# Optimization experiments

Measured on AMD Instinct MI355X. Metric: run time of the kernel, lower is better.

The kernel has to match this reference:

```python
import jax, jax.numpy as jnp
import numpy as np

B, L, M = 8192, 64, 64
LOCAL_DIM, MAX_UP, MAX_DN = 4, 64, 64


def setup_inputs() -> dict:
    key = jax.random.key(0)
    k1, k2 = jax.random.split(key)
    # occupation indices per site: 0=empty, 1=up, 2=down, 3=both
    indices = jax.random.randint(k1, (B, L), 0, LOCAL_DIM, dtype=jnp.int64)
    # learned GPS parameter tensor (local_dim, M, L, max_up+1, max_dn+1);
    # centered near 1 so the product over L sites stays numerically stable
    epsilon = 1.0 + 0.05 * jax.random.normal(
        k2, (LOCAL_DIM, M, L, MAX_UP + 1, MAX_DN + 1), dtype=jnp.float32)
    return {"indices": indices, "epsilon": epsilon}


def reference(indices, epsilon):
    b, l = indices.shape
    # cumulative particle counts of sites strictly before site i
    n_up = jnp.pad(jnp.cumsum(indices[:, :-1] & 1, axis=-1), ((0, 0), (1, 0)))
    n_dn = jnp.pad(jnp.cumsum((indices[:, :-1] & 2) // 2, axis=-1), ((0, 0), (1, 0)))
    site_ar = jnp.arange(l)[None, :]  # (1, L)
    # multi-axis gather: site_vals[b, i, m] = epsilon[idx[b,i], m, i, n_up[b,i], n_dn[b,i]]
    site_vals = epsilon[indices, :, site_ar, n_up, n_dn]  # (B, L, M)
    # product over sites, sum over GPS rank M
    log_psi = jnp.sum(jnp.prod(site_vals, axis=1), axis=-1)  # (B,)
    return log_psi
```

## Files before the change

### kernel.cpp

```cpp
#include <hip/hip_runtime.h>
#include <hip/hip_fp16.h>


#define TAB_HALF_BYTES ((size_t)89440 * 256 * 2)

__global__ __launch_bounds__(256) void seggps_transpose(
    const float* __restrict__ eps, __half* __restrict__ tab) {
  int bid = blockIdx.x;
  int d = bid / 2080;
  int t = bid % 2080;
  int l = (int)((sqrtf(8.0f * (float)t + 1.0f) - 1.0f) * 0.5f);
  while ((l + 1) * (l + 2) / 2 <= t) ++l;
  while (l * (l + 1) / 2 > t) --l;
  int u = t - l * (l + 1) / 2;

  int lane = threadIdx.x & 63;
  int wave = threadIdx.x >> 6;

  __shared__ float tile[64][65];

  const float* src = eps + ((size_t)(d * 64) * 64 + l) * 4225 + u * 65;
  if (lane <= l) {
#pragma unroll 4
    for (int m = wave; m < 64; m += 4) {
      tile[m][lane] = __builtin_nontemporal_load(&src[(size_t)m * 270400 + lane]);
    }
  }
  __syncthreads();

  int Pl = l * (l + 1) * (2 * l + 1) / 6;
  __half* dst = tab + (size_t)(Pl + u * (l + 1)) * 256 + d * 64 + lane;
#pragma unroll 4
  for (int n = wave; n <= l; n += 4) {
    dst[n * 256] = __float2half(tile[lane][n]);
  }
}

__global__ __launch_bounds__(256, 4) void seggps_main(
    const int* __restrict__ indices, const __half* __restrict__ tab,
    float* __restrict__ out) {
  int wave = threadIdx.x >> 6;
  int lane = threadIdx.x & 63;
  int b0 = (blockIdx.x * 4 + wave) * 2;

  int i0 = indices[b0 * 64 + lane];
  int i1 = indices[b0 * 64 + 64 + lane];

  float pa0 = 1.f, pb0 = 1.f, pa1 = 1.f, pb1 = 1.f;
  int up0 = 0, dn0 = 0, up1 = 0, dn1 = 0;
  int Pl = 0;
#pragma unroll 16
  for (int l = 0; l < 64; ++l) {
    int v0 = __shfl(i0, l, 64);
    int v1 = __shfl(i1, l, 64);
    int base = Pl * 256 + lane;
    int o0 = base + (up0 * (l + 1) + dn0) * 256 + v0 * 64;
    int o1 = base + (up1 * (l + 1) + dn1) * 256 + v1 * 64;
    float e0 = __half2float(tab[o0]);
    float e1 = __half2float(tab[o1]);
    if (l & 1) { pa0 *= e0; pa1 *= e1; }
    else       { pb0 *= e0; pb1 *= e1; }
    up0 += v0 & 1;  dn0 += (v0 >> 1) & 1;
    up1 += v1 & 1;  dn1 += (v1 >> 1) & 1;
    Pl += (l + 1) * (l + 1);
  }
  float p0 = pa0 * pb0;
  float p1 = pa1 * pb1;
#pragma unroll
  for (int s = 32; s; s >>= 1) {
    p0 += __shfl_down(p0, s, 64);
    p1 += __shfl_down(p1, s, 64);
  }
  if (lane == 0) {
    out[b0] = p0;
    out[b0 + 1] = p1;
  }
}

__global__ __launch_bounds__(256) void seggps_direct(
    const int* __restrict__ indices, const float* __restrict__ eps,
    float* __restrict__ out) {
  int wave = threadIdx.x >> 6;
  int lane = threadIdx.x & 63;
  int b = blockIdx.x * 4 + wave;

  int myidx = indices[b * 64 + lane];

  float p0 = 1.f, p1 = 1.f, p2 = 1.f, p3 = 1.f;
  int up = 0, dn = 0;
#pragma unroll 8
  for (int l = 0; l < 64; ++l) {
    int v = __shfl(myidx, l, 64);
    size_t off = ((size_t)((v * 64 + lane) * 64 + l)) * 4225 + up * 65 + dn;
    float e = eps[off];
    if ((l & 3) == 0)      p0 *= e;
    else if ((l & 3) == 1) p1 *= e;
    else if ((l & 3) == 2) p2 *= e;
    else                   p3 *= e;
    up += v & 1;
    dn += (v >> 1) & 1;
  }
  float p = (p0 * p1) * (p2 * p3);
#pragma unroll
  for (int s = 32; s; s >>= 1) p += __shfl_down(p, s, 64);
  if (lane == 0) out[b] = p;
}

extern "C" void kernel_launch(void* const* d_in, const int* in_sizes, int n_in,
                              void* d_out, int out_size, void* d_ws, size_t ws_size,
                              hipStream_t stream) {
  const int* indices = (const int*)d_in[0];
  const float* eps   = (const float*)d_in[1];
  float* out = (float*)d_out;

  if (ws_size >= TAB_HALF_BYTES) {
    __half* tab = (__half*)d_ws;
    hipLaunchKernelGGL(seggps_transpose, dim3(4 * 2080), dim3(256), 0, stream,
                       eps, tab);
    hipLaunchKernelGGL(seggps_main, dim3(8192 / 8), dim3(256), 0, stream,
                       indices, tab, out);
  } else {
    hipLaunchKernelGGL(seggps_direct, dim3(8192 / 4), dim3(256), 0, stream,
                       indices, eps, out);
  }
}
```

Before: 354.5 us.

## Restrict epsilon table transpose to particle-count ranges seen in the batch

```diff
diff --git a/kernel.cpp b/kernel.cpp
--- a/kernel.cpp
+++ b/kernel.cpp
@@ -4,8 +4,50 @@
 
 #define TAB_HALF_BYTES ((size_t)89440 * 256 * 2)
 
+__global__ __launch_bounds__(256) void seggps_init(int* __restrict__ ranges) {
+  int t = threadIdx.x;
+  if (t < 64) {
+    ranges[t] = 64;
+    ranges[64 + t] = -1;
+    ranges[128 + t] = 64;
+    ranges[192 + t] = -1;
+  }
+}
+
+__global__ __launch_bounds__(256) void seggps_ranges(
+    const int* __restrict__ indices, int* __restrict__ ranges) {
+  __shared__ int s_umin[64], s_umax[64], s_nmin[64], s_nmax[64];
+  int t = threadIdx.x;
+  if (t < 64) { s_umin[t] = 64; s_umax[t] = -1; s_nmin[t] = 64; s_nmax[t] = -1; }
+  __syncthreads();
+  int wave = t >> 6, lane = t & 63;
+  for (int i = 0; i < 16; ++i) {
+    int b = blockIdx.x * 64 + wave * 16 + i;
+    int v = indices[b * 64 + lane];
+    int up = v & 1, dn = (v >> 1) & 1;
+#pragma unroll
+    for (int s = 1; s < 64; s <<= 1) {
+      int au = __shfl_up(up, s, 64);
+      int ad = __shfl_up(dn, s, 64);
+      if (lane >= s) { up += au; dn += ad; }
+    }
+    int eu = up - (v & 1);
+    int ed = dn - ((v >> 1) & 1);
+    atomicMin(&s_umin[lane], eu); atomicMax(&s_umax[lane], eu);
+    atomicMin(&s_nmin[lane], ed); atomicMax(&s_nmax[lane], ed);
+  }
+  __syncthreads();
+  if (t < 64) {
+    atomicMin(&ranges[t], s_umin[t]);
+    atomicMax(&ranges[64 + t], s_umax[t]);
+    atomicMin(&ranges[128 + t], s_nmin[t]);
+    atomicMax(&ranges[192 + t], s_nmax[t]);
+  }
+}
+
 __global__ __launch_bounds__(256) void seggps_transpose(
-    const float* __restrict__ eps, __half* __restrict__ tab) {
+    const float* __restrict__ eps, __half* __restrict__ tab,
+    const int* __restrict__ ranges) {
   int bid = blockIdx.x;
   int d = bid / 2080;
   int t = bid % 2080;
@@ -14,13 +56,17 @@
   while (l * (l + 1) / 2 > t) --l;
   int u = t - l * (l + 1) / 2;
 
+  int umin = ranges[l], umax = ranges[64 + l];
+  if (u < umin || u > umax) return;
+  int nmin = ranges[128 + l], nmax = ranges[192 + l];
+
   int lane = threadIdx.x & 63;
   int wave = threadIdx.x >> 6;
 
   __shared__ float tile[64][65];
 
   const float* src = eps + ((size_t)(d * 64) * 64 + l) * 4225 + u * 65;
-  if (lane <= l) {
+  if (lane >= nmin && lane <= nmax) {
 #pragma unroll 4
     for (int m = wave; m < 64; m += 4) {
       tile[m][lane] = __builtin_nontemporal_load(&src[(size_t)m * 270400 + lane]);
@@ -30,8 +76,7 @@
 
   int Pl = l * (l + 1) * (2 * l + 1) / 6;
   __half* dst = tab + (size_t)(Pl + u * (l + 1)) * 256 + d * 64 + lane;
-#pragma unroll 4
-  for (int n = wave; n <= l; n += 4) {
+  for (int n = nmin + wave; n <= nmax; n += 4) {
     dst[n * 256] = __float2half(tile[lane][n]);
   }
 }
@@ -113,10 +158,14 @@
   const float* eps   = (const float*)d_in[1];
   float* out = (float*)d_out;
 
-  if (ws_size >= TAB_HALF_BYTES) {
+  if (ws_size >= TAB_HALF_BYTES + 1024) {
     __half* tab = (__half*)d_ws;
+    int* ranges = (int*)((char*)d_ws + TAB_HALF_BYTES);
+    hipLaunchKernelGGL(seggps_init, dim3(1), dim3(256), 0, stream, ranges);
+    hipLaunchKernelGGL(seggps_ranges, dim3(128), dim3(256), 0, stream,
+                       indices, ranges);
     hipLaunchKernelGGL(seggps_transpose, dim3(4 * 2080), dim3(256), 0, stream,
-                       eps, tab);
+                       eps, tab, ranges);
     hipLaunchKernelGGL(seggps_main, dim3(8192 / 8), dim3(256), 0, stream,
                        indices, tab, out);
   } else {
```

New measurement: 347.8 us. About the same (-1.9%).
